# Kernel optimization log

Hardware: AMD Instinct MI355X
Metric: run time of the kernel (lower is better)

## Reference

```python
import jax, jax.numpy as jnp
import numpy as np

B, L, HS, NWRD, NTGT, DIM = 8, 128, 1024, 32000, 2000, 128
EPS = 1e-12
T = 1.0  # eval temperature


def setup_inputs() -> dict:
    key = jax.random.key(0)
    ks = jax.random.split(key, 16)
    s = 0.02
    return {
        "inp_word": jax.random.randint(ks[0], (B, L), 0, NWRD, dtype=jnp.int32),
        "masks": jnp.ones((B, L), jnp.float32),
        "spt_mask": jax.random.randint(ks[1], (B, L), 0, 2, dtype=jnp.int32),
        "tgt_ids": jnp.sort(jax.random.randint(ks[2], (NTGT,), 0, NWRD, dtype=jnp.int32)),
        "ctx": jax.random.normal(ks[3], (B, L, HS), jnp.float32),
        "W_spt": jax.random.normal(ks[4], (HS, NTGT), jnp.float32) * s,
        "b_spt": jnp.zeros((NTGT,), jnp.float32),
        "W_nrm": jax.random.normal(ks[5], (HS, NWRD), jnp.float32) * s,
        "b_nrm": jnp.zeros((NWRD,), jnp.float32),
        "W_cpy": jax.random.normal(ks[6], (HS, HS), jnp.float32) * s,
        "b_cpy": jnp.zeros((HS,), jnp.float32),
        "word_emb": jax.random.normal(ks[7], (NWRD, DIM), jnp.float32) * s,
        "word_emb_tgt": jax.random.normal(ks[8], (NTGT, DIM), jnp.float32) * s,
        "g_spt": jax.random.gumbel(ks[9], (B, L, NTGT), jnp.float32),
        "g_nrm": jax.random.gumbel(ks[10], (B, L, NWRD + 1), jnp.float32),
    }


def reference(inp_word, masks, spt_mask, tgt_ids, ctx, W_spt, b_spt, W_nrm, b_nrm,
              W_cpy, b_cpy, word_emb, word_emb_tgt, g_spt, g_nrm):
    spt = spt_mask.astype(jnp.float32)                       # keyword tokens
    nrm = (1.0 - spt) * masks                                # normal (non-pad) tokens

    # special-token head: log(softmax + eps)
    pspt = jnp.log(jax.nn.softmax(jnp.einsum('blh,ht->blt', ctx, W_spt) + b_spt, axis=-1) + EPS)

    # normal head: vocab logits + self copy-attention score
    logits_nrm = jnp.einsum('blh,hv->blv', ctx, W_nrm) + b_nrm           # [B,L,NWRD]
    pcpy = jnp.einsum('blh,blh->bl', jnp.einsum('blh,hk->blk', ctx, W_cpy) + b_cpy, ctx)
    pnrm = jnp.log(jax.nn.softmax(jnp.concatenate([logits_nrm, pcpy[..., None]], axis=-1), axis=-1) + EPS)

    # gumbel-softmax relaxed samples
    sft_spt = jax.nn.softmax((pspt + g_spt) / T, axis=-1)    # [B,L,NTGT]
    sft_nrm = jax.nn.softmax((pnrm + g_nrm) / T, axis=-1)    # [B,L,NWRD+1]

    # hard word choices
    yspt = tgt_ids[jnp.argmax(sft_spt, axis=-1)]
    ynrm_raw = jnp.argmax(sft_nrm, axis=-1).astype(jnp.int32)
    ynrm = jnp.where(ynrm_raw == NWRD, inp_word, ynrm_raw)   # copy fallback
    obf_word = jnp.where(spt > 0, yspt, jnp.where(nrm > 0, ynrm, inp_word))

    # blended embeddings, scatter-combined per token group
    spt_emb = jnp.einsum('blt,td->bld', sft_spt, word_emb_tgt)
    nrm_emb = word_emb[inp_word] * sft_nrm[..., -1:] \
        + jnp.einsum('blv,vd->bld', sft_nrm[..., :-1], word_emb)
    base_emb = word_emb[obf_word]
    obf_word_emb = jnp.where(spt[..., None] > 0, spt_emb,
                             jnp.where(nrm[..., None] > 0, nrm_emb, base_emb))
    return obf_word_emb, obf_word, spt
```

## Files before the change

### kernel.cpp

```cpp
#include <hip/hip_runtime.h>
#include <math.h>

#define TOK   1024
#define HSZ   1024
#define DIM   128
#define NWRDC 32000
#define NTGTC 2000

typedef __attribute__((ext_vector_type(8))) short bf16x8;
typedef __attribute__((ext_vector_type(4))) float f32x4;

__device__ __forceinline__ ushort f2bf(float x) {
    union { float f; uint u; } c; c.f = x;
    return (ushort)((c.u + 0x7fffu + ((c.u >> 16) & 1u)) >> 16);
}
__device__ __forceinline__ float bf2f(ushort h) {
    union { uint u; float f; } c; c.u = ((uint)h) << 16;
    return c.f;
}
__device__ __forceinline__ uint4 pk8(const ushort v[8]) {
    uint4 u;
    u.x = (uint)v[0] | ((uint)v[1] << 16);
    u.y = (uint)v[2] | ((uint)v[3] << 16);
    u.z = (uint)v[4] | ((uint)v[5] << 16);
    u.w = (uint)v[6] | ((uint)v[7] << 16);
    return u;
}

#define GLL16(SRC, DST) __builtin_amdgcn_global_load_lds( \
    (const __attribute__((address_space(1))) void*)(SRC), \
    (__attribute__((address_space(3))) void*)(DST), 16, 0, 0)

__global__ __launch_bounds__(256) void split_ctx3(
    const float* __restrict__ x, ushort* __restrict__ hp,
    ushort* __restrict__ mp, ushort* __restrict__ lp)
{
    const int i4 = (blockIdx.x * 256 + threadIdx.x) * 4;
    float4 v = *(const float4*)(x + i4);
    float xs[4] = {v.x, v.y, v.z, v.w};
    ushort hh[4], mm[4], ll[4];
    #pragma unroll
    for (int k = 0; k < 4; ++k) {
        ushort h = f2bf(xs[k]);
        float r1 = xs[k] - bf2f(h);
        ushort m = f2bf(r1);
        ushort l = f2bf(r1 - bf2f(m));
        hh[k] = h; mm[k] = m; ll[k] = l;
    }
    uint2 u;
    u.x = (uint)hh[0] | ((uint)hh[1] << 16); u.y = (uint)hh[2] | ((uint)hh[3] << 16);
    *(uint2*)(hp + i4) = u;
    u.x = (uint)mm[0] | ((uint)mm[1] << 16); u.y = (uint)mm[2] | ((uint)mm[3] << 16);
    *(uint2*)(mp + i4) = u;
    u.x = (uint)ll[0] | ((uint)ll[1] << 16); u.y = (uint)ll[2] | ((uint)ll[3] << 16);
    *(uint2*)(lp + i4) = u;
}

__global__ __launch_bounds__(256, 2) void gemm_cpy(
    const ushort* __restrict__ ahi, const ushort* __restrict__ amd,
    const ushort* __restrict__ alo, const float* __restrict__ W,
    float* __restrict__ C)
{
    __shared__ __align__(16) ushort sm[30720];
    ushort* Ah = sm;
    ushort* Am = sm + 5120;
    ushort* Al = sm + 10240;
    ushort* Bh = sm + 15360;
    ushort* Bm = sm + 20480;
    ushort* Bl = sm + 25600;

    const int tid  = threadIdx.x;
    const int lane = tid & 63;
    const int fr   = lane & 15;
    const int fg   = lane >> 4;
    const int w    = tid >> 6;
    const int wrow = w >> 1;
    const int wcol = w & 1;
    const int t0   = blockIdx.x * 128;
    const int c0   = blockIdx.y * 128;

    const int arow = tid >> 2, akc = tid & 3;
    const int bcol = tid & 127, bkc0 = tid >> 7;

    f32x4 zero4 = {0.f, 0.f, 0.f, 0.f};
    f32x4 acc[4][4];
    #pragma unroll
    for (int i = 0; i < 4; ++i)
        #pragma unroll
        for (int j = 0; j < 4; ++j) acc[i][j] = zero4;

    for (int h0 = 0; h0 < HSZ; h0 += 32) {
        uint4 aH[2], aM[2], aL[2];
        float bx[2][8];
        #pragma unroll
        for (int rr = 0; rr < 2; ++rr) {
            const size_t so = (size_t)(t0 + arow + rr * 64) * HSZ + h0 + akc * 8;
            aH[rr] = *(const uint4*)(ahi + so);
            aM[rr] = *(const uint4*)(amd + so);
            aL[rr] = *(const uint4*)(alo + so);
        }
        #pragma unroll
        for (int rr = 0; rr < 2; ++rr) {
            const int kc = bkc0 + rr * 2;
            const float* wp = W + (size_t)(h0 + kc * 8) * HSZ + c0 + bcol;
            #pragma unroll
            for (int j = 0; j < 8; ++j) bx[rr][j] = wp[(size_t)j * HSZ];
        }
        __syncthreads();
        #pragma unroll
        for (int rr = 0; rr < 2; ++rr) {
            const int row = arow + rr * 64;
            *(uint4*)(Ah + row * 40 + akc * 8) = aH[rr];
            *(uint4*)(Am + row * 40 + akc * 8) = aM[rr];
            *(uint4*)(Al + row * 40 + akc * 8) = aL[rr];
        }
        #pragma unroll
        for (int rr = 0; rr < 2; ++rr) {
            const int kc = bkc0 + rr * 2;
            ushort hh[8], mm[8], ll[8];
            #pragma unroll
            for (int j = 0; j < 8; ++j) {
                float x = bx[rr][j];
                ushort h = f2bf(x);
                float r1 = x - bf2f(h);
                ushort m = f2bf(r1);
                hh[j] = h; mm[j] = m; ll[j] = f2bf(r1 - bf2f(m));
            }
            *(uint4*)(Bh + bcol * 40 + kc * 8) = pk8(hh);
            *(uint4*)(Bm + bcol * 40 + kc * 8) = pk8(mm);
            *(uint4*)(Bl + bcol * 40 + kc * 8) = pk8(ll);
        }
        __syncthreads();
        bf16x8 a1[4], a2[4], a3[4];
        #pragma unroll
        for (int i = 0; i < 4; ++i) {
            const int row = wrow * 64 + i * 16 + fr;
            a1[i] = *(const bf16x8*)(Ah + row * 40 + fg * 8);
            a2[i] = *(const bf16x8*)(Am + row * 40 + fg * 8);
            a3[i] = *(const bf16x8*)(Al + row * 40 + fg * 8);
        }
        #pragma unroll
        for (int j = 0; j < 4; ++j) {
            const int cr = wcol * 64 + j * 16 + fr;
            bf16x8 b1 = *(const bf16x8*)(Bh + cr * 40 + fg * 8);
            bf16x8 b2 = *(const bf16x8*)(Bm + cr * 40 + fg * 8);
            bf16x8 b3 = *(const bf16x8*)(Bl + cr * 40 + fg * 8);
            #pragma unroll
            for (int i = 0; i < 4; ++i) {
                acc[i][j] = __builtin_amdgcn_mfma_f32_16x16x32_bf16(a1[i], b1, acc[i][j], 0, 0, 0);
                acc[i][j] = __builtin_amdgcn_mfma_f32_16x16x32_bf16(a1[i], b2, acc[i][j], 0, 0, 0);
                acc[i][j] = __builtin_amdgcn_mfma_f32_16x16x32_bf16(a2[i], b1, acc[i][j], 0, 0, 0);
                acc[i][j] = __builtin_amdgcn_mfma_f32_16x16x32_bf16(a1[i], b3, acc[i][j], 0, 0, 0);
                acc[i][j] = __builtin_amdgcn_mfma_f32_16x16x32_bf16(a3[i], b1, acc[i][j], 0, 0, 0);
                acc[i][j] = __builtin_amdgcn_mfma_f32_16x16x32_bf16(a2[i], b2, acc[i][j], 0, 0, 0);
            }
        }
    }
    #pragma unroll
    for (int i = 0; i < 4; ++i)
        #pragma unroll
        for (int j = 0; j < 4; ++j)
            #pragma unroll
            for (int r = 0; r < 4; ++r) {
                const int trow = wrow * 64 + i * 16 + fg * 4 + r;
                const int dd   = wcol * 64 + j * 16 + fr;
                C[(size_t)(t0 + trow) * HSZ + c0 + dd] = acc[i][j][r];
            }
}

__global__ __launch_bounds__(256) void pcpy_dot(
    const float* __restrict__ C, const float* __restrict__ ctx,
    const float* __restrict__ bc, float* __restrict__ out)
{
    const int t = blockIdx.x, tid = threadIdx.x;
    const float4 c4 = *(const float4*)(C + (size_t)t * HSZ + tid * 4);
    const float4 x4 = *(const float4*)(ctx + (size_t)t * HSZ + tid * 4);
    const float4 b4 = *(const float4*)(bc + tid * 4);
    float p = (c4.x + b4.x) * x4.x + (c4.y + b4.y) * x4.y
            + (c4.z + b4.z) * x4.z + (c4.w + b4.w) * x4.w;
    #pragma unroll
    for (int off = 32; off > 0; off >>= 1) p += __shfl_down(p, off, 64);
    __shared__ float r4[4];
    if ((tid & 63) == 0) r4[tid >> 6] = p;
    __syncthreads();
    if (tid == 0) out[t] = r4[0] + r4[1] + r4[2] + r4[3];
}

__global__ __launch_bounds__(256, 2) void head_mfma(
    const ushort* __restrict__ ctx_hi, const ushort* __restrict__ ctx_lo,
    const float* __restrict__ W, const float* __restrict__ bias,
    const float* __restrict__ g, const float* __restrict__ emb,
    int V, int ldg, int tps, int n_tiles,
    float* __restrict__ wsW, float* __restrict__ wsBV,
    int* __restrict__ wsBI, float* __restrict__ wsE)
{
    __shared__ __align__(16) char smem[56320];
    ushort* Pl = (ushort*)smem;
    ushort* EM = (ushort*)(smem + 34816);
    float* sm_wsum = (float*)(smem + 53248);
    float* sm_bval = (float*)(smem + 54272);
    int*   sm_bidx = (int*)(smem + 55296);

    const int tid  = threadIdx.x;
    const int lane = tid & 63;
    const int fr   = lane & 15;
    const int fg   = lane >> 4;
    const int wv   = tid >> 6;
    const int wrow = wv >> 1;
    const int wcol = wv & 1;
    const int split = (int)blockIdx.x;
    const int t0    = (int)blockIdx.y * 128;

    if (tid < 128) {
        sm_wsum[tid * 2] = 0.f;        sm_wsum[tid * 2 + 1] = 0.f;
        sm_bval[tid * 2] = -INFINITY;  sm_bval[tid * 2 + 1] = -INFINITY;
        sm_bidx[tid * 2] = 0;          sm_bidx[tid * 2 + 1] = 0;
    }

    const int chunkRd  = (((fr & 1) << 2) | fg) ^ ((fr >> 1) & 7);
    const int laneAoff = wrow * 4096 + (fr >> 1) * 128 + chunkRd * 16;
    const int laneBoff = wcol * 4096 + (fr >> 1) * 128 + chunkRd * 16;

    const int cfA   = (lane & 7) ^ (lane >> 3);
    const int glTok = (wv * 8 + (lane >> 3)) * 2 + (cfA >> 2);
    const int glK   = (cfA & 3) * 8;
    const int glDst = wv * 1024;

    const int c4 = (tid & 31) * 4;
    const int hb = (tid >> 5) * 2;
    int wb01[4], wb23[4];
    #pragma unroll
    for (int i = 0; i < 4; ++i) {
        const int col = c4 + i;
        const int pair = col >> 1;
        const int ch01 = (((col & 1) << 2) | (hb >> 3)) ^ (pair & 7);
        const int ch23 = (((col & 1) << 2) | (2 + (hb >> 3))) ^ (pair & 7);
        wb01[i] = pair * 128 + ch01 * 16 + (hb & 7) * 2;
        wb23[i] = pair * 128 + ch23 * 16 + (hb & 7) * 2;
    }

    f32x4 zero4 = {0.f, 0.f, 0.f, 0.f};
    f32x4 Eacc[4][4];
    #pragma unroll
    for (int i = 0; i < 4; ++i)
        #pragma unroll
        for (int j = 0; j < 4; ++j) Eacc[i][j] = zero4;

    int tbeg = split * tps;
    int tend = tbeg + tps; if (tend > n_tiles) tend = n_tiles;

    #define STAGE_A(STEP, BASE) do {                                              \
        const size_t ro_ = (size_t)(t0 + glTok) * HSZ + (size_t)(STEP) * 32 + glK; \
        GLL16(ctx_hi + ro_,          (BASE) + glDst);                              \
        GLL16(ctx_hi + ro_ + 65536,  (BASE) + 4096 + glDst);                       \
        GLL16(ctx_lo + ro_,          (BASE) + 8192 + glDst);                       \
        GLL16(ctx_lo + ro_ + 65536,  (BASE) + 12288 + glDst);                      \
    } while (0)

    #define LOAD_W(STEP, VV) do {                                                 \
        const int gc_ = c0 + c4;                                                  \
        if (gc_ + 3 < V) {                                                        \
            const float* p_ = W + (size_t)((STEP) * 32 + hb) * V + gc_;           \
            VV[0] = *(const float4*)p_;                                           \
            VV[1] = *(const float4*)(p_ + V);                                     \
            VV[2] = *(const float4*)(p_ + 16 * (size_t)V);                        \
            VV[3] = *(const float4*)(p_ + 17 * (size_t)V);                        \
        } else {                                                                  \
            float4 z_ = {0.f, 0.f, 0.f, 0.f};                                     \
            VV[0] = z_; VV[1] = z_; VV[2] = z_; VV[3] = z_;                       \
        }                                                                         \
    } while (0)

    #define CONV_W(VV) do {                                                       \
        _Pragma("unroll")                                                         \
        for (int i_ = 0; i_ < 4; ++i_) {                                          \
            const float* fv0 = (const float*)&VV[0];                              \
            const float* fv1 = (const float*)&VV[1];                              \
            const float* fv2 = (const float*)&VV[2];                              \
            const float* fv3 = (const float*)&VV[3];                              \
            float a0 = fv0[i_], a1 = fv1[i_], a2 = fv2[i_], a3 = fv3[i_];         \
            ushort h0b = f2bf(a0); ushort l0b = f2bf(a0 - bf2f(h0b));             \
            ushort h1b = f2bf(a1); ushort l1b = f2bf(a1 - bf2f(h1b));             \
            ushort h2b = f2bf(a2); ushort l2b = f2bf(a2 - bf2f(h2b));             \
            ushort h3b = f2bf(a3); ushort l3b = f2bf(a3 - bf2f(h3b));             \
            *(uint*)(smem + 32768 + wb01[i_]) = (uint)h0b | ((uint)h1b << 16);    \
            *(uint*)(smem + 32768 + wb23[i_]) = (uint)h2b | ((uint)h3b << 16);    \
            *(uint*)(smem + 40960 + wb01[i_]) = (uint)l0b | ((uint)l1b << 16);    \
            *(uint*)(smem + 40960 + wb23[i_]) = (uint)l2b | ((uint)l3b << 16);    \
        }                                                                         \
    } while (0)

    for (int tt = tbeg; tt < tend; ++tt) {
        const int c0 = tt * 128;
        f32x4 acc[4][4];
        #pragma unroll
        for (int i = 0; i < 4; ++i)
            #pragma unroll
            for (int j = 0; j < 4; ++j) acc[i][j] = zero4;

        STAGE_A(0, smem);
        {
            float4 v0[4];
            LOAD_W(0, v0);
            CONV_W(v0);
        }
        __syncthreads();

        for (int ks = 0; ks < 32; ++ks) {
            const int cur = ks & 1;
            const bool more = (ks + 1) < 32;
            float4 vn[4];
            if (more) {
                STAGE_A(ks + 1, smem + (cur ^ 1) * 16384);
                LOAD_W(ks + 1, vn);
            }
            char* bA = smem + cur * 16384;
            bf16x8 ah[4], al[4];
            #pragma unroll
            for (int i = 0; i < 4; ++i) {
                ah[i] = *(const bf16x8*)(bA + laneAoff + i * 1024);
                al[i] = *(const bf16x8*)(bA + 8192 + laneAoff + i * 1024);
            }
            #pragma unroll
            for (int j = 0; j < 4; ++j) {
                bf16x8 vbh = *(const bf16x8*)(smem + 32768 + laneBoff + j * 1024);
                bf16x8 vbl = *(const bf16x8*)(smem + 40960 + laneBoff + j * 1024);
                #pragma unroll
                for (int i = 0; i < 4; ++i) {
                    acc[i][j] = __builtin_amdgcn_mfma_f32_16x16x32_bf16(ah[i], vbh, acc[i][j], 0, 0, 0);
                    acc[i][j] = __builtin_amdgcn_mfma_f32_16x16x32_bf16(ah[i], vbl, acc[i][j], 0, 0, 0);
                    acc[i][j] = __builtin_amdgcn_mfma_f32_16x16x32_bf16(al[i], vbh, acc[i][j], 0, 0, 0);
                }
            }
            __syncthreads();
            if (more) {
                CONV_W(vn);
            }
            __syncthreads();
        }

        float bias4[4];
        #pragma unroll
        for (int j = 0; j < 4; ++j) {
            const int gc = c0 + wcol * 64 + j * 16 + fr;
            bias4[j] = (gc < V) ? bias[gc] : 0.f;
        }
        #pragma unroll
        for (int i = 0; i < 4; ++i) {
            #pragma unroll
            for (int r = 0; r < 4; ++r) {
                const int trow = wrow * 64 + i * 16 + fg * 4 + r;
                const float* gp = g + (size_t)(t0 + trow) * ldg + c0 + wcol * 64 + fr;
                float esum = 0.f, mx = -INFINITY;
                int mi = 0;
                #pragma unroll
                for (int j = 0; j < 4; ++j) {
                    const int gc = c0 + wcol * 64 + j * 16 + fr;
                    float e = 0.f;
                    if (gc < V) {
                        const float s = acc[i][j][r] + bias4[j] + gp[j * 16];
                        e = __expf(s);
                        esum += e;
                        if (s > mx) { mx = s; mi = gc; }
                    }
                    Pl[trow * 136 + wcol * 64 + j * 16 + fr] = f2bf(e);
                }
                #pragma unroll
                for (int off = 1; off < 16; off <<= 1) {
                    const float ov = __shfl_xor(mx, off, 64);
                    const int   oi = __shfl_xor(mi, off, 64);
                    esum += __shfl_xor(esum, off, 64);
                    if (ov > mx || (ov == mx && oi < mi)) { mx = ov; mi = oi; }
                }
                if (fr == 0) {
                    sm_wsum[trow * 2 + wcol] += esum;
                    const float cb = sm_bval[trow * 2 + wcol];
                    const int   ci = sm_bidx[trow * 2 + wcol];
                    if (mx > cb || (mx == cb && mi < ci)) {
                        sm_bval[trow * 2 + wcol] = mx;
                        sm_bidx[trow * 2 + wcol] = mi;
                    }
                }
            }
        }

        #pragma unroll
        for (int hf = 0; hf < 2; ++hf) {
            __syncthreads();
            #pragma unroll
            for (int rr = 0; rr < 4; ++rr) {
                const int task = tid + rr * 256;
                const int d = task & 127;
                const int cc = task >> 7;
                ushort o8[8];
                #pragma unroll
                for (int j = 0; j < 8; ++j) {
                    const int gc = c0 + hf * 64 + cc * 8 + j;
                    o8[j] = (gc < V) ? f2bf(emb[(size_t)gc * DIM + d]) : (ushort)0;
                }
                *(uint4*)(EM + d * 72 + cc * 8) = pk8(o8);
            }
            __syncthreads();
            #pragma unroll
            for (int ksb = 0; ksb < 2; ++ksb) {
                bf16x8 ap[4];
                #pragma unroll
                for (int i = 0; i < 4; ++i) {
                    const int row = wrow * 64 + i * 16 + fr;
                    ap[i] = *(const bf16x8*)(Pl + row * 136 + hf * 64 + ksb * 32 + fg * 8);
                }
                #pragma unroll
                for (int j = 0; j < 4; ++j) {
                    const int dd = wcol * 64 + j * 16 + fr;
                    bf16x8 eb = *(const bf16x8*)(EM + dd * 72 + ksb * 32 + fg * 8);
                    #pragma unroll
                    for (int i = 0; i < 4; ++i)
                        Eacc[i][j] = __builtin_amdgcn_mfma_f32_16x16x32_bf16(ap[i], eb, Eacc[i][j], 0, 0, 0);
                }
            }
        }
        __syncthreads();
    }

    __syncthreads();
    if (tid < 128) {
        const float wsv = sm_wsum[tid * 2] + sm_wsum[tid * 2 + 1];
        const float b0 = sm_bval[tid * 2], b1 = sm_bval[tid * 2 + 1];
        const int   i0 = sm_bidx[tid * 2], i1 = sm_bidx[tid * 2 + 1];
        float bv; int bi;
        if (b0 > b1 || (b0 == b1 && i0 < i1)) { bv = b0; bi = i0; }
        else                                   { bv = b1; bi = i1; }
        const size_t o = (size_t)split * TOK + t0 + tid;
        wsW[o] = wsv; wsBV[o] = bv; wsBI[o] = bi;
    }
    #pragma unroll
    for (int i = 0; i < 4; ++i)
        #pragma unroll
        for (int j = 0; j < 4; ++j)
            #pragma unroll
            for (int r = 0; r < 4; ++r) {
                const int trow = wrow * 64 + i * 16 + fg * 4 + r;
                const int dd   = wcol * 64 + j * 16 + fr;
                wsE[((size_t)split * TOK + t0 + trow) * DIM + dd] = Eacc[i][j][r];
            }
}

__global__ __launch_bounds__(128) void combine_kernel(
    const int* __restrict__ inp_word, const float* __restrict__ masks,
    const int* __restrict__ spt_mask, const int* __restrict__ tgt_ids,
    const float* __restrict__ word_emb, const float* __restrict__ pcpy,
    const float* __restrict__ g_nrm,
    const float* __restrict__ nW, const float* __restrict__ nBV,
    const int* __restrict__ nBI, const float* __restrict__ nE, int NVn,
    const float* __restrict__ sW, const float* __restrict__ sBV,
    const int* __restrict__ sBI, const float* __restrict__ sE, int NVs,
    float* __restrict__ out)
{
    const int t = (int)blockIdx.x;
    const int d = (int)threadIdx.x;

    float Wn = 0.f, En = 0.f, bv = -INFINITY; int bi = 0;
    for (int v = 0; v < NVn; ++v) {
        const size_t o = (size_t)v * TOK + t;
        Wn += nW[o];
        En += nE[o * DIM + d];
        const float vv = nBV[o]; const int ii = nBI[o];
        if (vv > bv || (vv == bv && ii < bi)) { bv = vv; bi = ii; }
    }
    const int iw = inp_word[t];
    const float sc = pcpy[t] + g_nrm[(size_t)t * (NWRDC + 1) + NWRDC];
    const float ec = __expf(sc);
    Wn += ec;
    En += ec * word_emb[(size_t)iw * DIM + d];
    const int ynrm = (sc > bv) ? iw : bi;

    float Ws = 0.f, Ese = 0.f, sv = -INFINITY; int si = 0;
    for (int v = 0; v < NVs; ++v) {
        const size_t o = (size_t)v * TOK + t;
        Ws += sW[o];
        Ese += sE[o * DIM + d];
        const float vv = sBV[o]; const int ii = sBI[o];
        if (vv > sv || (vv == sv && ii < si)) { sv = vv; si = ii; }
    }
    const int yspt = tgt_ids[si];

    const float sptf = (float)spt_mask[t];
    const float nrmf = (1.f - sptf) * masks[t];

    float eo; int obf;
    if (sptf > 0.f)      { eo = Ese / Ws; obf = yspt; }
    else if (nrmf > 0.f) { eo = En / Wn;  obf = ynrm; }
    else                 { obf = iw; eo = word_emb[(size_t)iw * DIM + d]; }

    out[(size_t)t * DIM + d] = eo;
    if (d == 0) {
        out[(size_t)TOK * DIM + t]       = (float)obf;
        out[(size_t)TOK * DIM + TOK + t] = sptf;
    }
}

extern "C" void kernel_launch(void* const* d_in, const int* in_sizes, int n_in,
                              void* d_out, int out_size, void* d_ws, size_t ws_size,
                              hipStream_t stream)
{
    const int*   inp_word = (const int*)d_in[0];
    const float* masks    = (const float*)d_in[1];
    const int*   spt_mask = (const int*)d_in[2];
    const int*   tgt_ids  = (const int*)d_in[3];
    const float* ctx      = (const float*)d_in[4];
    const float* W_spt    = (const float*)d_in[5];
    const float* b_spt    = (const float*)d_in[6];
    const float* W_nrm    = (const float*)d_in[7];
    const float* b_nrm    = (const float*)d_in[8];
    const float* W_cpy    = (const float*)d_in[9];
    const float* b_cpy    = (const float*)d_in[10];
    const float* word_emb = (const float*)d_in[11];
    const float* word_emb_tgt = (const float*)d_in[12];
    const float* g_spt    = (const float*)d_in[13];
    const float* g_nrm    = (const float*)d_in[14];
    float* out = (float*)d_out;

    char* wsb = (char*)d_ws;
    float*  pcpy = (float*)wsb;
    ushort* ctxh = (ushort*)(wsb + 4096);
    ushort* ctxm = (ushort*)(wsb + 4096 + 2097152);
    ushort* ctxl = (ushort*)(wsb + 4096 + 4194304);
    char*   region = wsb + 4096 + 6291456;
    float*  Cws = (float*)region;

    const size_t per_split = (size_t)TOK * (DIM + 3) * 4;
    size_t avail = (ws_size > 6295552) ? (ws_size - 6295552) / per_split : 0;
    int NVn, NVs;
    if      (avail >= 72) { NVn = 64; NVs = 8; }
    else if (avail >= 56) { NVn = 48; NVs = 8; }
    else if (avail >= 40) { NVn = 32; NVs = 8; }
    else if (avail >= 24) { NVn = 16; NVs = 8; }
    else if (avail >= 12) { NVn = 8;  NVs = 4; }
    else if (avail >= 3)  { NVn = (int)avail - 1; NVs = 1; }
    else                  { NVn = 1;  NVs = 1; }

    float* nW  = (float*)region;
    float* nBV = nW + (size_t)NVn * TOK;
    int*   nBI = (int*)(nBV + (size_t)NVn * TOK);
    float* nE  = (float*)(nBI + (size_t)NVn * TOK);
    float* sW  = nE + (size_t)NVn * TOK * DIM;
    float* sBV = sW + (size_t)NVs * TOK;
    int*   sBI = (int*)(sBV + (size_t)NVs * TOK);
    float* sE  = (float*)(sBI + (size_t)NVs * TOK);

    const int ntile_n = NWRDC / 128;
    const int tps_n = (ntile_n + NVn - 1) / NVn;
    const int ntile_s = (NTGTC + 127) / 128;
    const int tps_s = (ntile_s + NVs - 1) / NVs;

    split_ctx3<<<dim3(TOK * HSZ / 1024), dim3(256), 0, stream>>>(ctx, ctxh, ctxm, ctxl);
    gemm_cpy<<<dim3(8, 8), dim3(256), 0, stream>>>(ctxh, ctxm, ctxl, W_cpy, Cws);
    pcpy_dot<<<dim3(TOK), dim3(256), 0, stream>>>(Cws, ctx, b_cpy, pcpy);
    head_mfma<<<dim3(NVn, 8), dim3(256), 0, stream>>>(
        ctxh, ctxm, W_nrm, b_nrm, g_nrm, word_emb, NWRDC, NWRDC + 1,
        tps_n, ntile_n, nW, nBV, nBI, nE);
    head_mfma<<<dim3(NVs, 8), dim3(256), 0, stream>>>(
        ctxh, ctxm, W_spt, b_spt, g_spt, word_emb_tgt, NTGTC, NTGTC,
        tps_s, ntile_s, sW, sBV, sBI, sE);
    combine_kernel<<<dim3(TOK), dim3(128), 0, stream>>>(
        inp_word, masks, spt_mask, tgt_ids, word_emb, pcpy, g_nrm,
        nW, nBV, nBI, nE, NVn, sW, sBV, sBI, sE, NVs, out);
    (void)in_sizes; (void)n_in; (void)out_size;
}
```

Before: 827.7 us.

## Fuse copy GEMM and both vocab heads into one persistent mega kernel

Merges the copy-score GEMM, its dot-product reduction, and both vocab head kernels into a single launch that picks its role by block index. The copy GEMM now reduces against ctx in its epilogue and writes per-column-block partial scores, which the combine kernel sums. The head body gains a double-buffered W tile in LDS, which removes one barrier per k-step. It also adds a revised LDS swizzle, a cheaper truncation-based hi/lo split of W, and s_setprio around the MFMA section. Split counts are now derived from workspace size, which adds LDS use (about 67KB per block) and could lower occupancy.

```diff
diff --git a/kernel.cpp b/kernel.cpp
--- a/kernel.cpp
+++ b/kernel.cpp
@@ -56,137 +56,8 @@
     *(uint2*)(lp + i4) = u;
 }
 
-__global__ __launch_bounds__(256, 2) void gemm_cpy(
-    const ushort* __restrict__ ahi, const ushort* __restrict__ amd,
-    const ushort* __restrict__ alo, const float* __restrict__ W,
-    float* __restrict__ C)
-{
-    __shared__ __align__(16) ushort sm[30720];
-    ushort* Ah = sm;
-    ushort* Am = sm + 5120;
-    ushort* Al = sm + 10240;
-    ushort* Bh = sm + 15360;
-    ushort* Bm = sm + 20480;
-    ushort* Bl = sm + 25600;
-
-    const int tid  = threadIdx.x;
-    const int lane = tid & 63;
-    const int fr   = lane & 15;
-    const int fg   = lane >> 4;
-    const int w    = tid >> 6;
-    const int wrow = w >> 1;
-    const int wcol = w & 1;
-    const int t0   = blockIdx.x * 128;
-    const int c0   = blockIdx.y * 128;
-
-    const int arow = tid >> 2, akc = tid & 3;
-    const int bcol = tid & 127, bkc0 = tid >> 7;
-
-    f32x4 zero4 = {0.f, 0.f, 0.f, 0.f};
-    f32x4 acc[4][4];
-    #pragma unroll
-    for (int i = 0; i < 4; ++i)
-        #pragma unroll
-        for (int j = 0; j < 4; ++j) acc[i][j] = zero4;
-
-    for (int h0 = 0; h0 < HSZ; h0 += 32) {
-        uint4 aH[2], aM[2], aL[2];
-        float bx[2][8];
-        #pragma unroll
-        for (int rr = 0; rr < 2; ++rr) {
-            const size_t so = (size_t)(t0 + arow + rr * 64) * HSZ + h0 + akc * 8;
-            aH[rr] = *(const uint4*)(ahi + so);
-            aM[rr] = *(const uint4*)(amd + so);
-            aL[rr] = *(const uint4*)(alo + so);
-        }
-        #pragma unroll
-        for (int rr = 0; rr < 2; ++rr) {
-            const int kc = bkc0 + rr * 2;
-            const float* wp = W + (size_t)(h0 + kc * 8) * HSZ + c0 + bcol;
-            #pragma unroll
-            for (int j = 0; j < 8; ++j) bx[rr][j] = wp[(size_t)j * HSZ];
-        }
-        __syncthreads();
-        #pragma unroll
-        for (int rr = 0; rr < 2; ++rr) {
-            const int row = arow + rr * 64;
-            *(uint4*)(Ah + row * 40 + akc * 8) = aH[rr];
-            *(uint4*)(Am + row * 40 + akc * 8) = aM[rr];
-            *(uint4*)(Al + row * 40 + akc * 8) = aL[rr];
-        }
-        #pragma unroll
-        for (int rr = 0; rr < 2; ++rr) {
-            const int kc = bkc0 + rr * 2;
-            ushort hh[8], mm[8], ll[8];
-            #pragma unroll
-            for (int j = 0; j < 8; ++j) {
-                float x = bx[rr][j];
-                ushort h = f2bf(x);
-                float r1 = x - bf2f(h);
-                ushort m = f2bf(r1);
-                hh[j] = h; mm[j] = m; ll[j] = f2bf(r1 - bf2f(m));
-            }
-            *(uint4*)(Bh + bcol * 40 + kc * 8) = pk8(hh);
-            *(uint4*)(Bm + bcol * 40 + kc * 8) = pk8(mm);
-            *(uint4*)(Bl + bcol * 40 + kc * 8) = pk8(ll);
-        }
-        __syncthreads();
-        bf16x8 a1[4], a2[4], a3[4];
-        #pragma unroll
-        for (int i = 0; i < 4; ++i) {
-            const int row = wrow * 64 + i * 16 + fr;
-            a1[i] = *(const bf16x8*)(Ah + row * 40 + fg * 8);
-            a2[i] = *(const bf16x8*)(Am + row * 40 + fg * 8);
-            a3[i] = *(const bf16x8*)(Al + row * 40 + fg * 8);
-        }
-        #pragma unroll
-        for (int j = 0; j < 4; ++j) {
-            const int cr = wcol * 64 + j * 16 + fr;
-            bf16x8 b1 = *(const bf16x8*)(Bh + cr * 40 + fg * 8);
-            bf16x8 b2 = *(const bf16x8*)(Bm + cr * 40 + fg * 8);
-            bf16x8 b3 = *(const bf16x8*)(Bl + cr * 40 + fg * 8);
-            #pragma unroll
-            for (int i = 0; i < 4; ++i) {
-                acc[i][j] = __builtin_amdgcn_mfma_f32_16x16x32_bf16(a1[i], b1, acc[i][j], 0, 0, 0);
-                acc[i][j] = __builtin_amdgcn_mfma_f32_16x16x32_bf16(a1[i], b2, acc[i][j], 0, 0, 0);
-                acc[i][j] = __builtin_amdgcn_mfma_f32_16x16x32_bf16(a2[i], b1, acc[i][j], 0, 0, 0);
-                acc[i][j] = __builtin_amdgcn_mfma_f32_16x16x32_bf16(a1[i], b3, acc[i][j], 0, 0, 0);
-                acc[i][j] = __builtin_amdgcn_mfma_f32_16x16x32_bf16(a3[i], b1, acc[i][j], 0, 0, 0);
-                acc[i][j] = __builtin_amdgcn_mfma_f32_16x16x32_bf16(a2[i], b2, acc[i][j], 0, 0, 0);
-            }
-        }
-    }
-    #pragma unroll
-    for (int i = 0; i < 4; ++i)
-        #pragma unroll
-        for (int j = 0; j < 4; ++j)
-            #pragma unroll
-            for (int r = 0; r < 4; ++r) {
-                const int trow = wrow * 64 + i * 16 + fg * 4 + r;
-                const int dd   = wcol * 64 + j * 16 + fr;
-                C[(size_t)(t0 + trow) * HSZ + c0 + dd] = acc[i][j][r];
-            }
-}
-
-__global__ __launch_bounds__(256) void pcpy_dot(
-    const float* __restrict__ C, const float* __restrict__ ctx,
-    const float* __restrict__ bc, float* __restrict__ out)
-{
-    const int t = blockIdx.x, tid = threadIdx.x;
-    const float4 c4 = *(const float4*)(C + (size_t)t * HSZ + tid * 4);
-    const float4 x4 = *(const float4*)(ctx + (size_t)t * HSZ + tid * 4);
-    const float4 b4 = *(const float4*)(bc + tid * 4);
-    float p = (c4.x + b4.x) * x4.x + (c4.y + b4.y) * x4.y
-            + (c4.z + b4.z) * x4.z + (c4.w + b4.w) * x4.w;
-    #pragma unroll
-    for (int off = 32; off > 0; off >>= 1) p += __shfl_down(p, off, 64);
-    __shared__ float r4[4];
-    if ((tid & 63) == 0) r4[tid >> 6] = p;
-    __syncthreads();
-    if (tid == 0) out[t] = r4[0] + r4[1] + r4[2] + r4[3];
-}
-
-__global__ __launch_bounds__(256, 2) void head_mfma(
+__device__ __forceinline__ void head_body(
+    char* smem, int b, int NVx,
     const ushort* __restrict__ ctx_hi, const ushort* __restrict__ ctx_lo,
     const float* __restrict__ W, const float* __restrict__ bias,
     const float* __restrict__ g, const float* __restrict__ emb,
@@ -194,12 +65,11 @@
     float* __restrict__ wsW, float* __restrict__ wsBV,
     int* __restrict__ wsBI, float* __restrict__ wsE)
 {
-    __shared__ __align__(16) char smem[56320];
     ushort* Pl = (ushort*)smem;
     ushort* EM = (ushort*)(smem + 34816);
-    float* sm_wsum = (float*)(smem + 53248);
-    float* sm_bval = (float*)(smem + 54272);
-    int*   sm_bidx = (int*)(smem + 55296);
+    float* sm_wsum = (float*)(smem + 65536);
+    float* sm_bval = (float*)(smem + 66560);
+    int*   sm_bidx = (int*)(smem + 67584);
 
     const int tid  = threadIdx.x;
     const int lane = tid & 63;
@@ -208,8 +78,8 @@
     const int wv   = tid >> 6;
     const int wrow = wv >> 1;
     const int wcol = wv & 1;
-    const int split = (int)blockIdx.x;
-    const int t0    = (int)blockIdx.y * 128;
+    const int split = b % NVx;
+    const int t0    = (b / NVx) * 128;
 
     if (tid < 128) {
         sm_wsum[tid * 2] = 0.f;        sm_wsum[tid * 2 + 1] = 0.f;
@@ -217,26 +87,29 @@
         sm_bidx[tid * 2] = 0;          sm_bidx[tid * 2 + 1] = 0;
     }
 
-    const int chunkRd  = (((fr & 1) << 2) | fg) ^ ((fr >> 1) & 7);
-    const int laneAoff = wrow * 4096 + (fr >> 1) * 128 + chunkRd * 16;
-    const int laneBoff = wcol * 4096 + (fr >> 1) * 128 + chunkRd * 16;
-
-    const int cfA   = (lane & 7) ^ (lane >> 3);
-    const int glTok = (wv * 8 + (lane >> 3)) * 2 + (cfA >> 2);
-    const int glK   = (cfA & 3) * 8;
+    const int chunkRd0 = (((fr & 1) << 2) | fg) ^ ((fr >> 1) & 7);
+    int aRd[4], bRd[4];
+    #pragma unroll
+    for (int i = 0; i < 4; ++i) {
+        aRd[i] = wrow * 4096 + i * 1024 + (fr >> 1) * 128 + ((chunkRd0 ^ i) << 4);
+        bRd[i] = wcol * 4096 + i * 1024 + (fr >> 1) * 128 + ((chunkRd0 ^ i) << 4);
+    }
+
+    const int v_    = (lane & 7) ^ (lane >> 3) ^ (wv & 3);
+    const int glTok = (wv * 8 + (lane >> 3)) * 2 + (v_ >> 2);
+    const int glK   = (v_ & 3) * 8;
     const int glDst = wv * 1024;
 
     const int c4 = (tid & 31) * 4;
-    const int hb = (tid >> 5) * 2;
-    int wb01[4], wb23[4];
+    const int hq = tid >> 5;
+    const int kc_w = hq >> 1, half_w = hq & 1;
+    int wOff[4];
     #pragma unroll
     for (int i = 0; i < 4; ++i) {
         const int col = c4 + i;
         const int pair = col >> 1;
-        const int ch01 = (((col & 1) << 2) | (hb >> 3)) ^ (pair & 7);
-        const int ch23 = (((col & 1) << 2) | (2 + (hb >> 3))) ^ (pair & 7);
-        wb01[i] = pair * 128 + ch01 * 16 + (hb & 7) * 2;
-        wb23[i] = pair * 128 + ch23 * 16 + (hb & 7) * 2;
+        const int ch = (((col & 1) << 2) | kc_w) ^ (pair & 7) ^ ((pair >> 3) & 3);
+        wOff[i] = pair * 128 + ch * 16 + half_w * 8;
     }
 
     f32x4 zero4 = {0.f, 0.f, 0.f, 0.f};
@@ -249,7 +122,7 @@
     int tbeg = split * tps;
     int tend = tbeg + tps; if (tend > n_tiles) tend = n_tiles;
 
-    #define STAGE_A(STEP, BASE) do {                                              \
+    #define STAGE_A(STEP, BASE) do {                                               \
         const size_t ro_ = (size_t)(t0 + glTok) * HSZ + (size_t)(STEP) * 32 + glK; \
         GLL16(ctx_hi + ro_,          (BASE) + glDst);                              \
         GLL16(ctx_hi + ro_ + 65536,  (BASE) + 4096 + glDst);                       \
@@ -258,36 +131,38 @@
     } while (0)
 
     #define LOAD_W(STEP, VV) do {                                                 \
-        const int gc_ = c0 + c4;                                                  \
-        if (gc_ + 3 < V) {                                                        \
-            const float* p_ = W + (size_t)((STEP) * 32 + hb) * V + gc_;           \
-            VV[0] = *(const float4*)p_;                                           \
-            VV[1] = *(const float4*)(p_ + V);                                     \
-            VV[2] = *(const float4*)(p_ + 16 * (size_t)V);                        \
-            VV[3] = *(const float4*)(p_ + 17 * (size_t)V);                        \
-        } else {                                                                  \
-            float4 z_ = {0.f, 0.f, 0.f, 0.f};                                     \
-            VV[0] = z_; VV[1] = z_; VV[2] = z_; VV[3] = z_;                       \
-        }                                                                         \
+        const int gc_ = c0 + c4;                                                   \
+        if (gc_ < V) {                                                             \
+            const float* p_ = W + (size_t)((STEP) * 32 + hq * 4) * V + gc_;        \
+            VV[0] = *(const float4*)p_;                                            \
+            VV[1] = *(const float4*)(p_ + V);                                      \
+            VV[2] = *(const float4*)(p_ + 2 * (size_t)V);                          \
+            VV[3] = *(const float4*)(p_ + 3 * (size_t)V);                          \
+        } else {                                                                   \
+            float4 z_ = {0.f, 0.f, 0.f, 0.f};                                      \
+            VV[0] = z_; VV[1] = z_; VV[2] = z_; VV[3] = z_;                        \
+        }                                                                          \
     } while (0)
 
-    #define CONV_W(VV) do {                                                       \
-        _Pragma("unroll")                                                         \
-        for (int i_ = 0; i_ < 4; ++i_) {                                          \
-            const float* fv0 = (const float*)&VV[0];                              \
-            const float* fv1 = (const float*)&VV[1];                              \
-            const float* fv2 = (const float*)&VV[2];                              \
-            const float* fv3 = (const float*)&VV[3];                              \
-            float a0 = fv0[i_], a1 = fv1[i_], a2 = fv2[i_], a3 = fv3[i_];         \
-            ushort h0b = f2bf(a0); ushort l0b = f2bf(a0 - bf2f(h0b));             \
-            ushort h1b = f2bf(a1); ushort l1b = f2bf(a1 - bf2f(h1b));             \
-            ushort h2b = f2bf(a2); ushort l2b = f2bf(a2 - bf2f(h2b));             \
-            ushort h3b = f2bf(a3); ushort l3b = f2bf(a3 - bf2f(h3b));             \
-            *(uint*)(smem + 32768 + wb01[i_]) = (uint)h0b | ((uint)h1b << 16);    \
-            *(uint*)(smem + 32768 + wb23[i_]) = (uint)h2b | ((uint)h3b << 16);    \
-            *(uint*)(smem + 40960 + wb01[i_]) = (uint)l0b | ((uint)l1b << 16);    \
-            *(uint*)(smem + 40960 + wb23[i_]) = (uint)l2b | ((uint)l3b << 16);    \
-        }                                                                         \
+    #define CONV_W(BH, BL, VV) do {                                               \
+        _Pragma("unroll")                                                          \
+        for (int i_ = 0; i_ < 4; ++i_) {                                           \
+            ushort h_[4], l_[4];                                                   \
+            _Pragma("unroll")                                                      \
+            for (int q_ = 0; q_ < 4; ++q_) {                                       \
+                float x_ = ((const float*)&VV[q_])[i_];                            \
+                union { float f; uint u; } c_; c_.f = x_;                          \
+                h_[q_] = (ushort)(c_.u >> 16);                                     \
+                union { uint u; float f; } t_; t_.u = c_.u & 0xFFFF0000u;          \
+                l_[q_] = f2bf(x_ - t_.f);                                          \
+            }                                                                      \
+            uint2 uh_ = {(uint)h_[0] | ((uint)h_[1] << 16),                        \
+                         (uint)h_[2] | ((uint)h_[3] << 16)};                       \
+            uint2 ul_ = {(uint)l_[0] | ((uint)l_[1] << 16),                        \
+                         (uint)l_[2] | ((uint)l_[3] << 16)};                       \
+            *(uint2*)((BH) + wOff[i_]) = uh_;                                      \
+            *(uint2*)((BL) + wOff[i_]) = ul_;                                      \
+        }                                                                          \
     } while (0)
 
     for (int tt = tbeg; tt < tend; ++tt) {
@@ -302,7 +177,7 @@
         {
             float4 v0[4];
             LOAD_W(0, v0);
-            CONV_W(v0);
+            CONV_W(smem + 32768, smem + 40960, v0);
         }
         __syncthreads();
 
@@ -315,16 +190,18 @@
                 LOAD_W(ks + 1, vn);
             }
             char* bA = smem + cur * 16384;
+            char* bB = smem + 32768 + cur * 16384;
             bf16x8 ah[4], al[4];
             #pragma unroll
             for (int i = 0; i < 4; ++i) {
-                ah[i] = *(const bf16x8*)(bA + laneAoff + i * 1024);
-                al[i] = *(const bf16x8*)(bA + 8192 + laneAoff + i * 1024);
-            }
+                ah[i] = *(const bf16x8*)(bA + aRd[i]);
+                al[i] = *(const bf16x8*)(bA + 8192 + aRd[i]);
+            }
+            __builtin_amdgcn_s_setprio(1);
             #pragma unroll
             for (int j = 0; j < 4; ++j) {
-                bf16x8 vbh = *(const bf16x8*)(smem + 32768 + laneBoff + j * 1024);
-                bf16x8 vbl = *(const bf16x8*)(smem + 40960 + laneBoff + j * 1024);
+                bf16x8 vbh = *(const bf16x8*)(bB + bRd[j]);
+                bf16x8 vbl = *(const bf16x8*)(bB + 8192 + bRd[j]);
                 #pragma unroll
                 for (int i = 0; i < 4; ++i) {
                     acc[i][j] = __builtin_amdgcn_mfma_f32_16x16x32_bf16(ah[i], vbh, acc[i][j], 0, 0, 0);
@@ -332,9 +209,10 @@
                     acc[i][j] = __builtin_amdgcn_mfma_f32_16x16x32_bf16(al[i], vbh, acc[i][j], 0, 0, 0);
                 }
             }
-            __syncthreads();
+            __builtin_amdgcn_s_setprio(0);
             if (more) {
-                CONV_W(vn);
+                char* nB = smem + 32768 + (cur ^ 1) * 16384;
+                CONV_W(nB, nB + 8192, vn);
             }
             __syncthreads();
         }
@@ -443,12 +321,176 @@
                 const int dd   = wcol * 64 + j * 16 + fr;
                 wsE[((size_t)split * TOK + t0 + trow) * DIM + dd] = Eacc[i][j][r];
             }
+    #undef STAGE_A
+    #undef LOAD_W
+    #undef CONV_W
+}
+
+__device__ __forceinline__ void cpy_body(
+    char* smemc, int cb,
+    const ushort* __restrict__ ahi, const ushort* __restrict__ amd,
+    const ushort* __restrict__ alo, const float* __restrict__ Wc,
+    const float* __restrict__ ctx, const float* __restrict__ bc,
+    float* __restrict__ pcpyP)
+{
+    ushort* sm = (ushort*)smemc;
+    ushort* Ah = sm;
+    ushort* Am = sm + 5120;
+    ushort* Al = sm + 10240;
+    ushort* Bh = sm + 15360;
+    ushort* Bm = sm + 20480;
+    ushort* Bl = sm + 25600;
+
+    const int tid  = threadIdx.x;
+    const int lane = tid & 63;
+    const int fr   = lane & 15;
+    const int fg   = lane >> 4;
+    const int w    = tid >> 6;
+    const int wrow = w >> 1;
+    const int wcol = w & 1;
+    const int t0   = (cb >> 3) * 128;
+    const int c0   = (cb & 7) * 128;
+
+    const int arow = tid >> 2, akc = tid & 3;
+    const int bcol = tid & 127, bkc0 = tid >> 7;
+
+    f32x4 zero4 = {0.f, 0.f, 0.f, 0.f};
+    f32x4 acc[4][4];
+    #pragma unroll
+    for (int i = 0; i < 4; ++i)
+        #pragma unroll
+        for (int j = 0; j < 4; ++j) acc[i][j] = zero4;
+
+    for (int h0 = 0; h0 < HSZ; h0 += 32) {
+        uint4 aH[2], aM[2], aL[2];
+        float bx[2][8];
+        #pragma unroll
+        for (int rr = 0; rr < 2; ++rr) {
+            const size_t so = (size_t)(t0 + arow + rr * 64) * HSZ + h0 + akc * 8;
+            aH[rr] = *(const uint4*)(ahi + so);
+            aM[rr] = *(const uint4*)(amd + so);
+            aL[rr] = *(const uint4*)(alo + so);
+        }
+        #pragma unroll
+        for (int rr = 0; rr < 2; ++rr) {
+            const int kc = bkc0 + rr * 2;
+            const float* wp = Wc + (size_t)(h0 + kc * 8) * HSZ + c0 + bcol;
+            #pragma unroll
+            for (int j = 0; j < 8; ++j) bx[rr][j] = wp[(size_t)j * HSZ];
+        }
+        __syncthreads();
+        #pragma unroll
+        for (int rr = 0; rr < 2; ++rr) {
+            const int row = arow + rr * 64;
+            *(uint4*)(Ah + row * 40 + akc * 8) = aH[rr];
+            *(uint4*)(Am + row * 40 + akc * 8) = aM[rr];
+            *(uint4*)(Al + row * 40 + akc * 8) = aL[rr];
+        }
+        #pragma unroll
+        for (int rr = 0; rr < 2; ++rr) {
+            const int kc = bkc0 + rr * 2;
+            ushort hh[8], mm[8], ll[8];
+            #pragma unroll
+            for (int j = 0; j < 8; ++j) {
+                float x = bx[rr][j];
+                ushort h = f2bf(x);
+                float r1 = x - bf2f(h);
+                ushort m = f2bf(r1);
+                hh[j] = h; mm[j] = m; ll[j] = f2bf(r1 - bf2f(m));
+            }
+            *(uint4*)(Bh + bcol * 40 + kc * 8) = pk8(hh);
+            *(uint4*)(Bm + bcol * 40 + kc * 8) = pk8(mm);
+            *(uint4*)(Bl + bcol * 40 + kc * 8) = pk8(ll);
+        }
+        __syncthreads();
+        bf16x8 a1[4], a2[4], a3[4];
+        #pragma unroll
+        for (int i = 0; i < 4; ++i) {
+            const int row = wrow * 64 + i * 16 + fr;
+            a1[i] = *(const bf16x8*)(Ah + row * 40 + fg * 8);
+            a2[i] = *(const bf16x8*)(Am + row * 40 + fg * 8);
+            a3[i] = *(const bf16x8*)(Al + row * 40 + fg * 8);
+        }
+        #pragma unroll
+        for (int j = 0; j < 4; ++j) {
+            const int cr = wcol * 64 + j * 16 + fr;
+            bf16x8 b1 = *(const bf16x8*)(Bh + cr * 40 + fg * 8);
+            bf16x8 b2 = *(const bf16x8*)(Bm + cr * 40 + fg * 8);
+            bf16x8 b3 = *(const bf16x8*)(Bl + cr * 40 + fg * 8);
+            #pragma unroll
+            for (int i = 0; i < 4; ++i) {
+                acc[i][j] = __builtin_amdgcn_mfma_f32_16x16x32_bf16(a1[i], b1, acc[i][j], 0, 0, 0);
+                acc[i][j] = __builtin_amdgcn_mfma_f32_16x16x32_bf16(a1[i], b2, acc[i][j], 0, 0, 0);
+                acc[i][j] = __builtin_amdgcn_mfma_f32_16x16x32_bf16(a2[i], b1, acc[i][j], 0, 0, 0);
+                acc[i][j] = __builtin_amdgcn_mfma_f32_16x16x32_bf16(a1[i], b3, acc[i][j], 0, 0, 0);
+                acc[i][j] = __builtin_amdgcn_mfma_f32_16x16x32_bf16(a3[i], b1, acc[i][j], 0, 0, 0);
+                acc[i][j] = __builtin_amdgcn_mfma_f32_16x16x32_bf16(a2[i], b2, acc[i][j], 0, 0, 0);
+            }
+        }
+    }
+
+    __syncthreads();
+    float* red = (float*)smemc;
+    float bb[4];
+    #pragma unroll
+    for (int j = 0; j < 4; ++j) bb[j] = bc[c0 + wcol * 64 + j * 16 + fr];
+    #pragma unroll
+    for (int i = 0; i < 4; ++i) {
+        #pragma unroll
+        for (int r = 0; r < 4; ++r) {
+            const int trow = wrow * 64 + i * 16 + fg * 4 + r;
+            const float* cx = ctx + (size_t)(t0 + trow) * HSZ + c0;
+            float s = 0.f;
+            #pragma unroll
+            for (int j = 0; j < 4; ++j) {
+                const int dd = wcol * 64 + j * 16 + fr;
+                s += (acc[i][j][r] + bb[j]) * cx[dd];
+            }
+            #pragma unroll
+            for (int off = 1; off < 16; off <<= 1) s += __shfl_xor(s, off, 64);
+            if (fr == 0) red[trow * 2 + wcol] = s;
+        }
+    }
+    __syncthreads();
+    if (tid < 128)
+        pcpyP[(size_t)(cb & 7) * TOK + t0 + tid] = red[tid * 2] + red[tid * 2 + 1];
+}
+
+__global__ __launch_bounds__(256, 2) void mega_kernel(
+    const ushort* __restrict__ ctxh, const ushort* __restrict__ ctxm,
+    const ushort* __restrict__ ctxl,
+    const float* __restrict__ W_nrm, const float* __restrict__ b_nrm,
+    const float* __restrict__ g_nrm, const float* __restrict__ word_emb,
+    const float* __restrict__ W_spt, const float* __restrict__ b_spt,
+    const float* __restrict__ g_spt, const float* __restrict__ word_emb_tgt,
+    const float* __restrict__ W_cpy, const float* __restrict__ b_cpy,
+    const float* __restrict__ ctx, float* __restrict__ pcpyP,
+    int NVn, int tps_n, int NVs, int tps_s,
+    float* __restrict__ nW, float* __restrict__ nBV, int* __restrict__ nBI,
+    float* __restrict__ nE,
+    float* __restrict__ sW, float* __restrict__ sBV, int* __restrict__ sBI,
+    float* __restrict__ sE)
+{
+    __shared__ __align__(16) char smem[68608];
+    const int bid = (int)blockIdx.x;
+    const int nbn = NVn * 8, nbs = NVs * 8;
+    if (bid < nbn) {
+        head_body(smem, bid, NVn, ctxh, ctxm, W_nrm, b_nrm, g_nrm, word_emb,
+                  NWRDC, NWRDC + 1, tps_n, NWRDC / 128, nW, nBV, nBI, nE);
+    } else if (bid < nbn + nbs) {
+        head_body(smem, bid - nbn, NVs, ctxh, ctxm, W_spt, b_spt, g_spt,
+                  word_emb_tgt, NTGTC, NTGTC, tps_s, (NTGTC + 127) / 128,
+                  sW, sBV, sBI, sE);
+    } else {
+        cpy_body(smem, bid - nbn - nbs, ctxh, ctxm, ctxl, W_cpy, ctx, b_cpy,
+                 pcpyP);
+    }
 }
 
 __global__ __launch_bounds__(128) void combine_kernel(
     const int* __restrict__ inp_word, const float* __restrict__ masks,
     const int* __restrict__ spt_mask, const int* __restrict__ tgt_ids,
-    const float* __restrict__ word_emb, const float* __restrict__ pcpy,
+    const float* __restrict__ word_emb, const float* __restrict__ pcpyP,
     const float* __restrict__ g_nrm,
     const float* __restrict__ nW, const float* __restrict__ nBV,
     const int* __restrict__ nBI, const float* __restrict__ nE, int NVn,
@@ -467,8 +509,12 @@
         const float vv = nBV[o]; const int ii = nBI[o];
         if (vv > bv || (vv == bv && ii < bi)) { bv = vv; bi = ii; }
     }
+    float pc = 0.f;
+    #pragma unroll
+    for (int y = 0; y < 8; ++y) pc += pcpyP[(size_t)y * TOK + t];
+
     const int iw = inp_word[t];
-    const float sc = pcpy[t] + g_nrm[(size_t)t * (NWRDC + 1) + NWRDC];
+    const float sc = pc + g_nrm[(size_t)t * (NWRDC + 1) + NWRDC];
     const float ec = __expf(sc);
     Wn += ec;
     En += ec * word_emb[(size_t)iw * DIM + d];
@@ -521,23 +567,22 @@
     float* out = (float*)d_out;
 
     char* wsb = (char*)d_ws;
-    float*  pcpy = (float*)wsb;
-    ushort* ctxh = (ushort*)(wsb + 4096);
-    ushort* ctxm = (ushort*)(wsb + 4096 + 2097152);
-    ushort* ctxl = (ushort*)(wsb + 4096 + 4194304);
-    char*   region = wsb + 4096 + 6291456;
-    float*  Cws = (float*)region;
-
+    float*  pcpyP = (float*)wsb;
+    ushort* ctxh = (ushort*)(wsb + 32768);
+    ushort* ctxm = ctxh + 1048576;
+    ushort* ctxl = ctxm + 1048576;
+    char*   region = wsb + 32768 + 6291456;
+    const size_t base = 32768 + 6291456;
     const size_t per_split = (size_t)TOK * (DIM + 3) * 4;
-    size_t avail = (ws_size > 6295552) ? (ws_size - 6295552) / per_split : 0;
-    int NVn, NVs;
-    if      (avail >= 72) { NVn = 64; NVs = 8; }
-    else if (avail >= 56) { NVn = 48; NVs = 8; }
-    else if (avail >= 40) { NVn = 32; NVs = 8; }
-    else if (avail >= 24) { NVn = 16; NVs = 8; }
-    else if (avail >= 12) { NVn = 8;  NVs = 4; }
-    else if (avail >= 3)  { NVn = (int)avail - 1; NVs = 1; }
-    else                  { NVn = 1;  NVs = 1; }
+
+    size_t navail = (ws_size > base + 2 * per_split)
+                        ? (ws_size - base) / per_split : 2;
+    int NVs = (int)(navail / 5);
+    if (NVs < 1) NVs = 1; if (NVs > 8) NVs = 8;
+    long rem = (long)navail - NVs;
+    int NVn;
+    if (rem >= 8) { NVn = (int)(rem & ~7L); if (NVn > 64) NVn = 64; }
+    else          { NVn = (rem < 1) ? 1 : (int)rem; }
 
     float* nW  = (float*)region;
     float* nBV = nW + (size_t)NVn * TOK;
@@ -548,22 +593,17 @@
     int*   sBI = (int*)(sBV + (size_t)NVs * TOK);
     float* sE  = (float*)(sBI + (size_t)NVs * TOK);
 
-    const int ntile_n = NWRDC / 128;
-    const int tps_n = (ntile_n + NVn - 1) / NVn;
+    const int tps_n = (NWRDC / 128 + NVn - 1) / NVn;
     const int ntile_s = (NTGTC + 127) / 128;
     const int tps_s = (ntile_s + NVs - 1) / NVs;
 
     split_ctx3<<<dim3(TOK * HSZ / 1024), dim3(256), 0, stream>>>(ctx, ctxh, ctxm, ctxl);
-    gemm_cpy<<<dim3(8, 8), dim3(256), 0, stream>>>(ctxh, ctxm, ctxl, W_cpy, Cws);
-    pcpy_dot<<<dim3(TOK), dim3(256), 0, stream>>>(Cws, ctx, b_cpy, pcpy);
-    head_mfma<<<dim3(NVn, 8), dim3(256), 0, stream>>>(
-        ctxh, ctxm, W_nrm, b_nrm, g_nrm, word_emb, NWRDC, NWRDC + 1,
-        tps_n, ntile_n, nW, nBV, nBI, nE);
-    head_mfma<<<dim3(NVs, 8), dim3(256), 0, stream>>>(
-        ctxh, ctxm, W_spt, b_spt, g_spt, word_emb_tgt, NTGTC, NTGTC,
-        tps_s, ntile_s, sW, sBV, sBI, sE);
+    mega_kernel<<<dim3(NVn * 8 + NVs * 8 + 64), dim3(256), 0, stream>>>(
+        ctxh, ctxm, ctxl, W_nrm, b_nrm, g_nrm, word_emb,
+        W_spt, b_spt, g_spt, word_emb_tgt, W_cpy, b_cpy, ctx, pcpyP,
+        NVn, tps_n, NVs, tps_s, nW, nBV, nBI, nE, sW, sBV, sBI, sE);
     combine_kernel<<<dim3(TOK), dim3(128), 0, stream>>>(
-        inp_word, masks, spt_mask, tgt_ids, word_emb, pcpy, g_nrm,
+        inp_word, masks, spt_mask, tgt_ids, word_emb, pcpyP, g_nrm,
         nW, nBV, nBI, nE, NVn, sW, sBV, sBI, sE, NVs, out);
     (void)in_sizes; (void)n_in; (void)out_size;
 }
```

Result: slower. 946.0 us (+14.3%).
